# Optimization experiments

Measured on AMD Instinct MI355X. Metric: run time of the kernel, lower is better.

The kernel has to match this reference:

```python
import jax, jax.numpy as jnp
import numpy as np

EPS = 1e-5

def _ln(x, g, b):
    m = jnp.mean(x, axis=-1, keepdims=True)
    v = jnp.var(x, axis=-1, keepdims=True)
    return (x - m) / jnp.sqrt(v + EPS) * g + b

def _mha(q, k, v, Wqkv, bqkv, Wo, bo, nh):
    # torch nn.MultiheadAttention with packed in_proj: rows [0:D]=Q, [D:2D]=K, [2D:3D]=V
    D = q.shape[-1]; hd = D // nh
    qp = q @ Wqkv[:D].T + bqkv[:D]
    kp = k @ Wqkv[D:2 * D].T + bqkv[D:2 * D]
    vp = v @ Wqkv[2 * D:].T + bqkv[2 * D:]
    sh = lambda t: t.reshape(t.shape[0], t.shape[1], nh, hd).transpose(0, 2, 1, 3)
    scores = jnp.einsum('bhqd,bhkd->bhqk', sh(qp), sh(kp)) / np.float32(np.sqrt(hd))
    a = jax.nn.softmax(scores, axis=-1)
    o = jnp.einsum('bhqk,bhkd->bhqd', a, sh(vp)).transpose(0, 2, 1, 3).reshape(q.shape[0], q.shape[1], D)
    return o @ Wo.T + bo

def _forward(x, W_in, b_in, W_l, b_l, g_l, be_l, W_ih, W_hh, b_ih, b_hh, mem0,
             W_rh, b_rh, W_wh, b_wh, W_eh, b_eh, W_rg, b_rg, W_wg, b_wg,
             W_wm_qkv, b_wm_qkv, W_wm_o, b_wm_o, W_ca_qkv, b_ca_qkv, W_ca_o, b_ca_o,
             W_ai, b_ai, g_ca, be_ca, W_out, b_out):
    B, S, _ = x.shape
    H = W_in.shape[0]
    # input projection + residual MLP stack (eval mode: dropout is identity)
    h = x @ W_in.T + b_in
    for i in range(W_l.shape[0]):
        r = h
        h = _ln(jax.nn.relu(h @ W_l[i].T + b_l[i]), g_l[i], be_l[i])
        h = h + r  # use_residual=True
    # working-memory (NTM-style) scan over time
    Hd = H

    def step(carry, xt):
        hs, cs, mem = carry
        gates = xt @ W_ih.T + b_ih + hs @ W_hh.T + b_hh
        i_, f_, g_, o_ = jnp.split(gates, 4, axis=-1)  # torch LSTM gate order i,f,g,o
        cs = jax.nn.sigmoid(f_) * cs + jax.nn.sigmoid(i_) * jnp.tanh(g_)
        hs = jax.nn.sigmoid(o_) * jnp.tanh(cs)
        # read (attention over memory, then gate)
        rk = hs @ W_rh.T + b_rh
        ro = _mha(rk[:, None, :], mem, mem, W_wm_qkv, b_wm_qkv, W_wm_o, b_wm_o, 4)
        rg = jax.nn.sigmoid(hs @ W_rg.T + b_rg)  # [B,1]
        read = (rg[:, :, None] * ro)[:, 0]
        # write (erase + add with content-based addressing, unscaled bmm softmax)
        wp = hs @ W_wh.T + b_wh
        wk, wv = wp[:, :Hd], wp[:, Hd:]
        ev = jax.nn.sigmoid(hs @ W_eh.T + b_eh)
        wg = jax.nn.sigmoid(hs @ W_wg.T + b_wg)  # [B,1]
        att = jax.nn.softmax(jnp.einsum('bd,bmd->bm', wk, mem), axis=-1)
        ew = att[:, :, None]  # [B,M,1]
        mem = mem * (1.0 - ew * ev[:, None, :]) + wg[:, None, :] * (ew * wv[:, None, :])
        return (hs, cs, mem), xt + read

    mem_init = jnp.broadcast_to(mem0, (B,) + mem0.shape)
    init = (jnp.zeros((B, H), x.dtype), jnp.zeros((B, H), x.dtype), mem_init)
    _, outs = jax.lax.scan(step, init, h.transpose(1, 0, 2))
    wm = outs.transpose(1, 0, 2)  # [B,S,H]
    # cognitive attention, task_type='general' (no task modulation branch)
    att = _mha(wm, wm, wm, W_ca_qkv, b_ca_qkv, W_ca_o, b_ca_o, 8)
    inten = jax.nn.sigmoid(wm @ W_ai.T + b_ai)
    co = _ln(att * inten + wm, g_ca, be_ca)
    return co @ W_out.T + b_out

def setup_inputs():
    key = jax.random.key(0)
    ks = iter(jax.random.split(key, 40))
    B, S, DI, H, DO, L, M = 16, 512, 64, 128, 64, 3, 32
    w = lambda *s: jax.random.normal(next(ks), s, jnp.float32) * 0.05
    d = {}
    d['x'] = jax.random.normal(next(ks), (B, S, DI), jnp.float32)
    d['W_in'] = w(H, DI); d['b_in'] = jnp.zeros(H)
    d['W_l'] = w(L, H, H); d['b_l'] = jnp.zeros((L, H))
    d['g_l'] = jnp.ones((L, H)); d['be_l'] = jnp.zeros((L, H))
    d['W_ih'] = w(4 * H, H); d['W_hh'] = w(4 * H, H)
    d['b_ih'] = jnp.zeros(4 * H); d['b_hh'] = jnp.zeros(4 * H)
    d['mem0'] = w(M, H)
    d['W_rh'] = w(H, H); d['b_rh'] = jnp.zeros(H)
    d['W_wh'] = w(2 * H, H); d['b_wh'] = jnp.zeros(2 * H)
    d['W_eh'] = w(H, H); d['b_eh'] = jnp.zeros(H)
    d['W_rg'] = w(1, H); d['b_rg'] = jnp.zeros(1)
    d['W_wg'] = w(1, H); d['b_wg'] = jnp.zeros(1)
    d['W_wm_qkv'] = w(3 * H, H); d['b_wm_qkv'] = jnp.zeros(3 * H)
    d['W_wm_o'] = w(H, H); d['b_wm_o'] = jnp.zeros(H)
    d['W_ca_qkv'] = w(3 * H, H); d['b_ca_qkv'] = jnp.zeros(3 * H)
    d['W_ca_o'] = w(H, H); d['b_ca_o'] = jnp.zeros(H)
    d['W_ai'] = w(1, H); d['b_ai'] = jnp.zeros(1)
    d['g_ca'] = jnp.ones(H); d['be_ca'] = jnp.zeros(H)
    d['W_out'] = w(DO, H); d['b_out'] = jnp.zeros(DO)
    return d

def reference(x, W_in, b_in, W_l, b_l, g_l, be_l, W_ih, W_hh, b_ih, b_hh, mem0,
              W_rh, b_rh, W_wh, b_wh, W_eh, b_eh, W_rg, b_rg, W_wg, b_wg,
              W_wm_qkv, b_wm_qkv, W_wm_o, b_wm_o, W_ca_qkv, b_ca_qkv, W_ca_o, b_ca_o,
              W_ai, b_ai, g_ca, be_ca, W_out, b_out):
    return _forward(x, W_in, b_in, W_l, b_l, g_l, be_l, W_ih, W_hh, b_ih, b_hh, mem0,
                    W_rh, b_rh, W_wh, b_wh, W_eh, b_eh, W_rg, b_rg, W_wg, b_wg,
                    W_wm_qkv, b_wm_qkv, W_wm_o, b_wm_o, W_ca_qkv, b_ca_qkv, W_ca_o, b_ca_o,
                    W_ai, b_ai, g_ca, be_ca, W_out, b_out)
```

## Files before the change

### kernel.cpp

```cpp
#include <hip/hip_runtime.h>
#include <hip/hip_bf16.h>


typedef short bf16x8 __attribute__((ext_vector_type(8)));
typedef float f32x4 __attribute__((ext_vector_type(4)));
typedef float f32x16 __attribute__((ext_vector_type(16)));

__device__ __forceinline__ float bl(uint u) { return __uint_as_float(u << 16); }
__device__ __forceinline__ float bh(uint u) { return __uint_as_float(u & 0xffff0000u); }
__device__ __forceinline__ float b2f(ushort u) { return __uint_as_float(((uint)u) << 16); }
__device__ __forceinline__ ushort f2b(float f) {
  uint u = __float_as_uint(f);
  u += 0x7fffu + ((u >> 16) & 1u);
  return (ushort)(u >> 16);
}
__device__ __forceinline__ uint cvtpk(float lo, float hi) {
  uint r;
  asm("v_cvt_pk_bf16_f32 %0, %1, %2" : "=v"(r) : "v"(lo), "v"(hi));
  return r;
}
__device__ __forceinline__ float rdl(float v, int lane) {
  return __int_as_float(__builtin_amdgcn_readlane(__float_as_int(v), lane));
}
__device__ __forceinline__ float sigm(float x) { return 1.0f / (1.0f + __expf(-x)); }
__device__ __forceinline__ float tanh_(float x) { float e = __expf(2.0f * x); return 1.0f - 2.0f / (e + 1.0f); }

__device__ __forceinline__ float dppror_add(float v, const int n) {
  int s;
  switch (n) {
    case 1: s = __builtin_amdgcn_update_dpp(0, __float_as_int(v), 0x121, 0xF, 0xF, true); break;
    case 2: s = __builtin_amdgcn_update_dpp(0, __float_as_int(v), 0x122, 0xF, 0xF, true); break;
    case 4: s = __builtin_amdgcn_update_dpp(0, __float_as_int(v), 0x124, 0xF, 0xF, true); break;
    default: s = __builtin_amdgcn_update_dpp(0, __float_as_int(v), 0x128, 0xF, 0xF, true); break;
  }
  return v + __int_as_float(s);
}
__device__ __forceinline__ float dppror_max(float v, const int n) {
  int s;
  switch (n) {
    case 1: s = __builtin_amdgcn_update_dpp(0, __float_as_int(v), 0x121, 0xF, 0xF, true); break;
    case 2: s = __builtin_amdgcn_update_dpp(0, __float_as_int(v), 0x122, 0xF, 0xF, true); break;
    case 4: s = __builtin_amdgcn_update_dpp(0, __float_as_int(v), 0x124, 0xF, 0xF, true); break;
    default: s = __builtin_amdgcn_update_dpp(0, __float_as_int(v), 0x128, 0xF, 0xF, true); break;
  }
  return fmaxf(v, __int_as_float(s));
}
__device__ __forceinline__ float swap16_add(float v) {
  int a = __float_as_int(v), b = a;
  asm("v_permlane16_swap_b32 %0, %1" : "+v"(a), "+v"(b));
  return __int_as_float(a) + __int_as_float(b);
}
__device__ __forceinline__ float swap16_max(float v) {
  int a = __float_as_int(v), b = a;
  asm("v_permlane16_swap_b32 %0, %1" : "+v"(a), "+v"(b));
  return fmaxf(__int_as_float(a), __int_as_float(b));
}
__device__ __forceinline__ float fold32_add(float v) {
  int a = __float_as_int(v), b = a;
  asm("v_permlane32_swap_b32 %0, %1" : "+v"(a), "+v"(b));
  return __int_as_float(a) + __int_as_float(b);
}
__device__ __forceinline__ float qx1(float v) {
  return __int_as_float(__builtin_amdgcn_update_dpp(0, __float_as_int(v), 0xB1, 0xF, 0xF, true));
}
__device__ __forceinline__ float qx2(float v) {
  return __int_as_float(__builtin_amdgcn_update_dpp(0, __float_as_int(v), 0x4E, 0xF, 0xF, true));
}

#define O_H     ((size_t)0)
#define O_GX    ((size_t)1048576)
#define O_EW    ((size_t)1048576)
#define O_QCA   ((size_t)1048576)
#define O_KCA   ((size_t)2097152)
#define O_VCA   ((size_t)3145728)
#define O_AO    ((size_t)4194304)
#define O_WHF   ((size_t)4194304)
#define O_HS    ((size_t)5242880)
#define O_WM    ((size_t)5242880)
#define O_ST    ((size_t)6291456)
#define O_Q     ((size_t)9437184)
#define O_WGS   ((size_t)10485760)
#define O_RGS   ((size_t)10493952)
#define O_BQC   ((size_t)10502144)
#define O_MEMA  ((size_t)10502272)
#define O_PWIN  ((size_t)27279488)
#define O_PWL   ((size_t)27283584)
#define O_PWIH  ((size_t)27308160)
#define O_PCMB  ((size_t)27340928)
#define O_PQKV  ((size_t)27373696)
#define O_PWOC  ((size_t)27398272)
#define O_PWOUT ((size_t)27406464)
#define O_PWOWM ((size_t)27410688)
#define O_WQC16 ((size_t)27418880)
#define O_CAN   ((size_t)27427072)

#define F4LD(DST, OFS, P) { float4 _f = *(const float4*)(P); DST[(OFS)]=_f.x; DST[(OFS)+1]=_f.y; DST[(OFS)+2]=_f.z; DST[(OFS)+3]=_f.w; }

struct CV { const void* src; uint dst; uint n; };
struct CVA { CV d[36]; };
__global__ __launch_bounds__(256) void k_cvt(CVA a, ushort* cb)
{
  __shared__ int flag;
  int tid = threadIdx.x;
  const ushort* xu = (const ushort*)a.d[0].src;
  if (tid < 64) {
    int sane = 0;
    for (int i = tid; i < 512; i += 64) {
      int e = (xu[2 * i] >> 7) & 0xFF;
      sane += (e >= 0x70 && e <= 0x8E) ? 1 : 0;
    }
#pragma unroll
    for (int d = 1; d < 64; d <<= 1) sane += __shfl_xor(sane, d, 64);
    if (tid == 0) flag = (sane > 256) ? 0 : 1;
  }
  __syncthreads();
  int isf32 = flag;
  CV c = a.d[blockIdx.x];
  ushort* dst = cb + c.dst;
  uint start = blockIdx.y * 256 + tid, stride = gridDim.y * 256;
  if (isf32) {
    const float* s = (const float*)c.src;
    for (uint j = start; j < c.n; j += stride) dst[j] = f2b(s[j]);
  } else {
    const ushort* s = (const ushort*)c.src;
    for (uint j = start; j < c.n; j += stride) dst[j] = s[j];
  }
}

__global__ __launch_bounds__(256) void k_wqcomb(const ushort* __restrict__ Wqkv, const ushort* __restrict__ Wrh,
                                                const ushort* __restrict__ brh, const ushort* __restrict__ bqkv,
                                                ushort* __restrict__ wqc, float* __restrict__ bqc)
{
  __shared__ float qr[2][128];
  int tid = threadIdx.x;
  int r = tid >> 7, e = tid & 127;
  int j = blockIdx.x * 2 + r;
  qr[r][e] = b2f(Wqkv[j * 128 + e]);
  __syncthreads();
  float acc = 0.f;
  for (int k = 0; k < 128; ++k) acc += qr[r][k] * b2f(Wrh[k * 128 + e]);
  wqc[j * 128 + e] = f2b(acc);
  if (e == 0) {
    float s = 0.f;
    for (int k = 0; k < 128; ++k) s += qr[r][k] * b2f(brh[k]);
    bqc[j] = s + b2f(bqkv[j]);
  }
}

struct PD { const ushort* src; uint* dst; int R, C2, RT, base; };
struct PA { PD d[12]; };
__global__ __launch_bounds__(256) void k_pack(PA a)
{
  int p = blockIdx.x >> 5, sl = blockIdx.x & 31;
  PD q = a.d[p];
  for (int d2 = sl; d2 < q.C2; d2 += 32)
    for (int j = threadIdx.x; j < q.R; j += 256)
      q.dst[(size_t)d2 * q.RT + q.base + j] = *(const uint*)(q.src + (size_t)j * q.C2 * 2 + d2 * 2);
}

__global__ __launch_bounds__(256) void k_whh(const ushort* __restrict__ Whh, float* __restrict__ whf)
{
  int e = blockIdx.x * 256 + threadIdx.x;
  int j = e & 127, th = e >> 7;
  int g = j >> 5, kk = j & 31, c = th >> 2, sl = th & 3;
  whf[e] = b2f(Whh[(g * 128 + c) * 128 + sl * 32 + kk]);
}

__device__ __forceinline__ void mlp_layer(float& h0, float& h1, const uint* wp, const float* bias, int li, int l)
{
  float t0 = bias[(1 + li) * 128 + l], t1 = bias[(1 + li) * 128 + 64 + l];
#pragma unroll
  for (int d2 = 0; d2 < 64; ++d2) {
    float s0 = rdl(d2 < 32 ? h0 : h1, (2 * d2) & 63);
    float s1 = rdl(d2 < 32 ? h0 : h1, (2 * d2 + 1) & 63);
    uint u0 = wp[d2 * 128 + l], u1 = wp[d2 * 128 + 64 + l];
    t0 += s0 * bl(u0) + s1 * bh(u0);
    t1 += s0 * bl(u1) + s1 * bh(u1);
  }
  t0 = fmaxf(t0, 0.f); t1 = fmaxf(t1, 0.f);
  float sm = t0 + t1, sq = t0 * t0 + t1 * t1;
#pragma unroll
  for (int d = 1; d < 64; d <<= 1) { sm += __shfl_xor(sm, d, 64); sq += __shfl_xor(sq, d, 64); }
  float mn = sm * 0.0078125f;
  float var = sq * 0.0078125f - mn * mn;
  float rstd = rsqrtf(var + 1e-5f);
  float ng0 = bias[(4 + li) * 128 + l], ng1 = bias[(4 + li) * 128 + 64 + l];
  float nb0 = bias[(7 + li) * 128 + l], nb1 = bias[(7 + li) * 128 + 64 + l];
  h0 = (t0 - mn) * rstd * ng0 + nb0 + h0;
  h1 = (t1 - mn) * rstd * ng1 + nb1 + h1;
}

__global__ __launch_bounds__(256, 1) void k_mlp(const ushort* __restrict__ x, const uint* __restrict__ pk,
    const ushort* __restrict__ b_in, const ushort* __restrict__ b_l, const ushort* __restrict__ g_l,
    const ushort* __restrict__ be_l, float* __restrict__ h_all)
{
  __shared__ uint lds[12288];
  __shared__ float bias[1280];
  int tid = threadIdx.x;
  for (int i = tid; i < 12288; i += 256) lds[i] = pk[i];
  for (int i = tid; i < 1280; i += 256) {
    int which = i >> 7, e = i & 127;
    float v;
    if (which == 0) v = b2f(b_in[e]);
    else if (which < 4) v = b2f(b_l[(which - 1) * 128 + e]);
    else if (which < 7) v = b2f(g_l[(which - 4) * 128 + e]);
    else v = b2f(be_l[(which - 7) * 128 + e]);
    bias[i] = v;
  }
  __syncthreads();
  int wv = tid >> 6, l = tid & 63;
  float h0a[8], h1a[8];
#pragma unroll
  for (int ps = 0; ps < 8; ++ps) {
    int tok = blockIdx.x * 32 + ps * 4 + wv;
    float xv = b2f(x[(size_t)tok * 64 + l]);
    float h0 = bias[l], h1 = bias[64 + l];
#pragma unroll
    for (int d2 = 0; d2 < 32; ++d2) {
      float s0 = rdl(xv, 2 * d2), s1 = rdl(xv, 2 * d2 + 1);
      uint u0 = lds[d2 * 128 + l], u1 = lds[d2 * 128 + 64 + l];
      h0 += s0 * bl(u0) + s1 * bh(u0);
      h1 += s0 * bl(u1) + s1 * bh(u1);
    }
    mlp_layer(h0, h1, lds + 4096, bias, 0, l);
    h0a[ps] = h0; h1a[ps] = h1;
  }
  __syncthreads();
  for (int i = tid; i < 8192; i += 256) lds[i] = pk[12288 + i];
  __syncthreads();
#pragma unroll
  for (int ps = 0; ps < 8; ++ps) {
    float h0 = h0a[ps], h1 = h1a[ps];
    mlp_layer(h0, h1, lds, bias, 1, l);
    h0a[ps] = h0; h1a[ps] = h1;
  }
  __syncthreads();
  for (int i = tid; i < 8192; i += 256) lds[i] = pk[20480 + i];
  __syncthreads();
#pragma unroll
  for (int ps = 0; ps < 8; ++ps) {
    int tok = blockIdx.x * 32 + ps * 4 + wv;
    float h0 = h0a[ps], h1 = h1a[ps];
    mlp_layer(h0, h1, lds, bias, 2, l);
    h_all[(size_t)tok * 128 + l] = h0;
    h_all[(size_t)tok * 128 + 64 + l] = h1;
  }
}

__global__ __launch_bounds__(256, 1) void k_gates(const float* __restrict__ h_all, const uint* __restrict__ pk,
    const ushort* __restrict__ b_ih, const ushort* __restrict__ b_hh, float* __restrict__ gx)
{
  __shared__ uint lds[8192];
  __shared__ float biasg[512];
  int tid = threadIdx.x;
  for (int i = tid; i < 512; i += 256) biasg[i] = b2f(b_ih[i]) + b2f(b_hh[i]);
  int wv = tid >> 6, l = tid & 63;
  for (int s = 0; s < 4; ++s) {
    __syncthreads();
    for (int i = tid; i < 8192; i += 256) { int d2 = i >> 7, j = i & 127; lds[i] = pk[d2 * 512 + s * 128 + j]; }
    __syncthreads();
    for (int ps = 0; ps < 8; ++ps) {
      int tok = blockIdx.x * 32 + ps * 4 + wv;
      float h0 = h_all[(size_t)tok * 128 + l], h1 = h_all[(size_t)tok * 128 + 64 + l];
      float a0 = biasg[s * 128 + l], a1 = biasg[s * 128 + 64 + l];
#pragma unroll
      for (int d2 = 0; d2 < 64; ++d2) {
        float s0 = rdl(d2 < 32 ? h0 : h1, (2 * d2) & 63);
        float s1 = rdl(d2 < 32 ? h0 : h1, (2 * d2 + 1) & 63);
        uint u0 = lds[d2 * 128 + l], u1 = lds[d2 * 128 + 64 + l];
        a0 += s0 * bl(u0) + s1 * bh(u0);
        a1 += s0 * bl(u1) + s1 * bh(u1);
      }
      gx[(size_t)tok * 512 + s * 128 + l] = a0;
      gx[(size_t)tok * 512 + s * 128 + 64 + l] = a1;
    }
  }
}

__global__ __launch_bounds__(512, 2) void k_lstm(const float* __restrict__ gx, const float* __restrict__ whf,
                                                 float* __restrict__ hs_all)
{
  __shared__ __align__(16) float hsl[2][128];
  int tid = threadIdx.x;
  int b = blockIdx.x;
  int s = tid & 3, c = tid >> 2;
  f32x16 wA, wB, wC, wD, wE, wF, wG, wH;
  {
    const float4* wp = (const float4*)(whf + (size_t)tid * 128);
    float4 a0, a1, a2, a3;
#define LW16(V, Q) \
    a0 = wp[(Q)]; a1 = wp[(Q) + 1]; a2 = wp[(Q) + 2]; a3 = wp[(Q) + 3]; \
    V[0]=a0.x; V[1]=a0.y; V[2]=a0.z; V[3]=a0.w; V[4]=a1.x; V[5]=a1.y; V[6]=a1.z; V[7]=a1.w; \
    V[8]=a2.x; V[9]=a2.y; V[10]=a2.z; V[11]=a2.w; V[12]=a3.x; V[13]=a3.y; V[14]=a3.z; V[15]=a3.w;
    LW16(wA, 0)  LW16(wB, 4)  LW16(wC, 8)  LW16(wD, 12)
    LW16(wE, 16) LW16(wF, 20) LW16(wG, 24) LW16(wH, 28)
#undef LW16
  }
  if (tid < 128) hsl[0][tid] = 0.f;
  float cs = 0.f;
  const float* gbase = gx + (size_t)b * 512 * 512 + s * 128 + c;
  float gcur = gbase[0];
  float* hout = hs_all + (size_t)b * 512 * 128 + c;
  __syncthreads();
  for (int t = 0; t < 512; ++t) {
    float gnext = 0.f;
    if (t < 511) gnext = gbase[(size_t)(t + 1) * 512];
    const float* hp = &hsl[t & 1][s * 32];
    float p0 = (s == 0) ? gcur : 0.f;
    float p1 = (s == 1) ? gcur : 0.f;
    float p2 = (s == 2) ? gcur : 0.f;
    float p3 = (s == 3) ? gcur : 0.f;
    float4 h4;
#define DOT4(V0, V1, V2, V3, J, HOFS) \
    h4 = *(const float4*)(hp + (HOFS)); \
    p0 = fmaf(V0[(J)+0], h4.x, p0); p0 = fmaf(V0[(J)+1], h4.y, p0); p0 = fmaf(V0[(J)+2], h4.z, p0); p0 = fmaf(V0[(J)+3], h4.w, p0); \
    p1 = fmaf(V1[(J)+0], h4.x, p1); p1 = fmaf(V1[(J)+1], h4.y, p1); p1 = fmaf(V1[(J)+2], h4.z, p1); p1 = fmaf(V1[(J)+3], h4.w, p1); \
    p2 = fmaf(V2[(J)+0], h4.x, p2); p2 = fmaf(V2[(J)+1], h4.y, p2); p2 = fmaf(V2[(J)+2], h4.z, p2); p2 = fmaf(V2[(J)+3], h4.w, p2); \
    p3 = fmaf(V3[(J)+0], h4.x, p3); p3 = fmaf(V3[(J)+1], h4.y, p3); p3 = fmaf(V3[(J)+2], h4.z, p3); p3 = fmaf(V3[(J)+3], h4.w, p3);
    DOT4(wA, wC, wE, wG, 0, 0)   DOT4(wA, wC, wE, wG, 4, 4)
    DOT4(wA, wC, wE, wG, 8, 8)   DOT4(wA, wC, wE, wG, 12, 12)
    DOT4(wB, wD, wF, wH, 0, 16)  DOT4(wB, wD, wF, wH, 4, 20)
    DOT4(wB, wD, wF, wH, 8, 24)  DOT4(wB, wD, wF, wH, 12, 28)
#undef DOT4
    p0 += qx1(p0); p0 += qx2(p0);
    p1 += qx1(p1); p1 += qx2(p1);
    p2 += qx1(p2); p2 += qx2(p2);
    p3 += qx1(p3); p3 += qx2(p3);
    cs = sigm(p1) * cs + sigm(p0) * tanh_(p2);
    float hv = sigm(p3) * tanh_(cs);
    if (s == 0) {
      hsl[(t + 1) & 1][c] = hv;
      hout[(size_t)t * 128] = hv;
    }
    gcur = gnext;
    __syncthreads();
  }
}

__global__ __launch_bounds__(256, 1) void k_proj(const float* __restrict__ hs_all, const uint* __restrict__ pk,
    const ushort* __restrict__ bwh, const ushort* __restrict__ beh, const float* __restrict__ bqc,
    const ushort* __restrict__ wrg, const ushort* __restrict__ brg, const ushort* __restrict__ wwg,
    const ushort* __restrict__ bwg,
    float* __restrict__ st, float* __restrict__ q_a, float* __restrict__ rg_a)
{
  __shared__ uint lds[8192];
  __shared__ float biasc[512];
  int tid = threadIdx.x;
  for (int i = tid; i < 512; i += 256)
    biasc[i] = (i < 256) ? b2f(bwh[i]) : (i < 384) ? b2f(beh[i - 256]) : bqc[i - 384];
  float brgv = b2f(brg[0]), bwgv = b2f(bwg[0]);
  int wv = tid >> 6, l = tid & 63;
  for (int s = 0; s < 4; ++s) {
    __syncthreads();
    for (int i = tid; i < 8192; i += 256) { int d2 = i >> 7, j = i & 127; lds[i] = pk[d2 * 512 + s * 128 + j]; }
    __syncthreads();
    for (int ps = 0; ps < 8; ++ps) {
      int tok = blockIdx.x * 32 + ps * 4 + wv;
      float h0 = hs_all[(size_t)tok * 128 + l], h1 = hs_all[(size_t)tok * 128 + 64 + l];
      float a0 = biasc[s * 128 + l], a1 = biasc[s * 128 + 64 + l];
#pragma unroll
      for (int d2 = 0; d2 < 64; ++d2) {
        float s0 = rdl(d2 < 32 ? h0 : h1, (2 * d2) & 63);
        float s1 = rdl(d2 < 32 ? h0 : h1, (2 * d2 + 1) & 63);
        uint u0 = lds[d2 * 128 + l], u1 = lds[d2 * 128 + 64 + l];
        a0 += s0 * bl(u0) + s1 * bh(u0);
        a1 += s0 * bl(u1) + s1 * bh(u1);
      }
      if (s == 0) {
        st[(size_t)tok * 384 + l] = a0;
        st[(size_t)tok * 384 + 64 + l] = a1;
        float pr = h0 * b2f(wrg[l]) + h1 * b2f(wrg[64 + l]);
#pragma unroll
        for (int d = 1; d < 64; d <<= 1) pr += __shfl_xor(pr, d, 64);
        if (l == 0) rg_a[tok] = sigm(pr + brgv);
      } else if (s == 1) {
        float pw = h0 * b2f(wwg[l]) + h1 * b2f(wwg[64 + l]);
#pragma unroll
        for (int d = 1; d < 64; d <<= 1) pw += __shfl_xor(pw, d, 64);
        float wg = sigm(pw + bwgv);
        st[(size_t)tok * 384 + 256 + l] = wg * a0;
        st[(size_t)tok * 384 + 256 + 64 + l] = wg * a1;
      } else if (s == 2) {
        st[(size_t)tok * 384 + 128 + l] = sigm(a0);
        st[(size_t)tok * 384 + 128 + 64 + l] = sigm(a1);
      } else {
        q_a[(size_t)tok * 128 + l] = a0;
        q_a[(size_t)tok * 128 + 64 + l] = a1;
      }
    }
  }
}

__global__ __launch_bounds__(64, 1) void k_memrec(const float* __restrict__ st, const ushort* __restrict__ mem0,
    float* __restrict__ ew_all)
{
  __shared__ __align__(16) float sbuf[2][384];
  int l = threadIdx.x;
  int b = blockIdx.x;
  int r = l & 31, h = l >> 5;
  f32x16 mA, mB, mC, mD;
  {
    const uint* m0 = (const uint*)mem0 + r * 64 + 32 * h;
    uint4 uq;
#define LD16(V, OFS) \
    uq = *(const uint4*)(m0 + (OFS)); \
    V[0]=bl(uq.x); V[1]=bh(uq.x); V[2]=bl(uq.y); V[3]=bh(uq.y); \
    V[4]=bl(uq.z); V[5]=bh(uq.z); V[6]=bl(uq.w); V[7]=bh(uq.w); \
    uq = *(const uint4*)(m0 + (OFS) + 4); \
    V[8]=bl(uq.x); V[9]=bh(uq.x); V[10]=bl(uq.y); V[11]=bh(uq.y); \
    V[12]=bl(uq.z); V[13]=bh(uq.z); V[14]=bl(uq.w); V[15]=bh(uq.w);
    LD16(mA, 0) LD16(mB, 8) LD16(mC, 16) LD16(mD, 24)
#undef LD16
  }
  const float* stb = st + (size_t)b * 512 * 384;
  {
    float4 a = *(const float4*)(stb + 4 * l);
    float2 c = *(const float2*)(stb + 256 + 2 * l);
    *(float4*)(&sbuf[0][4 * l]) = a;
    *(float2*)(&sbuf[0][256 + 2 * l]) = c;
  }
  float4 ga1 = *(const float4*)(stb + 384 + 4 * l);
  float2 gc1 = *(const float2*)(stb + 384 + 256 + 2 * l);
  float moff = 0.f;
  float* ewp = ew_all + (size_t)b * 512 * 32 + r;
  for (int t = 0; t < 512; ++t) {
    int cur = t & 1, nxt = cur ^ 1;
    float4 ga2 = make_float4(0.f, 0.f, 0.f, 0.f);
    float2 gc2 = make_float2(0.f, 0.f);
    if (t + 2 < 512) {
      const float* sp = stb + (size_t)(t + 2) * 384;
      ga2 = *(const float4*)(sp + 4 * l);
      gc2 = *(const float2*)(sp + 256 + 2 * l);
    }
    const float* wkp = &sbuf[cur][h * 64];
    float dx = 0.f, dy = 0.f, dz = 0.f, dw = 0.f;
    float4 w4;
#define DOT4(V, J0, OFS) \
    w4 = *(const float4*)(wkp + (OFS)); \
    dx = fmaf(w4.x, V[(J0)+0], dx); dy = fmaf(w4.y, V[(J0)+1], dy); \
    dz = fmaf(w4.z, V[(J0)+2], dz); dw = fmaf(w4.w, V[(J0)+3], dw);
    DOT4(mA, 0, 0)  DOT4(mA, 4, 4)  DOT4(mA, 8, 8)   DOT4(mA, 12, 12)
    DOT4(mB, 0, 16) DOT4(mB, 4, 20) DOT4(mB, 8, 24)  DOT4(mB, 12, 28)
    DOT4(mC, 0, 32) DOT4(mC, 4, 36) DOT4(mC, 8, 40)  DOT4(mC, 12, 44)
    DOT4(mD, 0, 48) DOT4(mD, 4, 52) DOT4(mD, 8, 56)  DOT4(mD, 12, 60)
#undef DOT4
    float dp = (dx + dy) + (dz + dw);
    dp = fold32_add(dp);
    float e = __expf(dp - moff);
    float s16 = dppror_add(dppror_add(dppror_add(dppror_add(e, 1), 2), 4), 8);
    float den = swap16_add(s16);
    float ew = e * __builtin_amdgcn_rcpf(den);
    float x16 = dppror_max(dppror_max(dppror_max(dppror_max(dp, 1), 2), 4), 8);
    const float* evp = &sbuf[cur][128 + h * 64];
    const float* gvp = &sbuf[cur][256 + h * 64];
    float4 e4, g4;
#define UPD4(V, J0, OFS) \
    e4 = *(const float4*)(evp + (OFS)); g4 = *(const float4*)(gvp + (OFS)); \
    V[(J0)+0] = fmaf(ew, fmaf(-e4.x, V[(J0)+0], g4.x), V[(J0)+0]); \
    V[(J0)+1] = fmaf(ew, fmaf(-e4.y, V[(J0)+1], g4.y), V[(J0)+1]); \
    V[(J0)+2] = fmaf(ew, fmaf(-e4.z, V[(J0)+2], g4.z), V[(J0)+2]); \
    V[(J0)+3] = fmaf(ew, fmaf(-e4.w, V[(J0)+3], g4.w), V[(J0)+3]);
    UPD4(mA, 0, 0)  UPD4(mA, 4, 4)  UPD4(mA, 8, 8)   UPD4(mA, 12, 12)
    UPD4(mB, 0, 16) UPD4(mB, 4, 20) UPD4(mB, 8, 24)  UPD4(mB, 12, 28)
    UPD4(mC, 0, 32) UPD4(mC, 4, 36) UPD4(mC, 8, 40)  UPD4(mC, 12, 44)
    UPD4(mD, 0, 48) UPD4(mD, 4, 52) UPD4(mD, 8, 56)  UPD4(mD, 12, 60)
#undef UPD4
    if (t < 511) {
      *(float4*)(&sbuf[nxt][4 * l]) = ga1;
      *(float2*)(&sbuf[nxt][256 + 2 * l]) = gc1;
    }
    ga1 = ga2; gc1 = gc2;
    if (l < 32) ewp[(size_t)t * 32] = ew;
    moff = swap16_max(x16);
  }
}

__global__ __launch_bounds__(256, 1) void k_snap(const float* __restrict__ st, const float* __restrict__ ew_all,
    const ushort* __restrict__ mem0, uint* __restrict__ mem_all)
{
  int b = blockIdx.x >> 3;
  int j = ((blockIdx.x & 7) << 8) + threadIdx.x;
  int m = j >> 6, d2 = j & 63;
  uint u0 = ((const uint*)mem0)[(m << 6) + d2];
  float s0 = bl(u0), s1 = bh(u0);
  const float* ep = st + (size_t)b * 512 * 384 + 128 + 2 * d2;
  const float* gp = ep + 128;
  const float* ap = ew_all + (size_t)b * 512 * 32 + m;
  uint* mb = mem_all + (size_t)b * 512 * 2048 + (m << 6) + d2;
  for (int t = 0; t < 512; t += 4) {
    float2 eA = *(const float2*)(ep + (size_t)(t + 0) * 384);
    float2 eB = *(const float2*)(ep + (size_t)(t + 1) * 384);
    float2 eC = *(const float2*)(ep + (size_t)(t + 2) * 384);
    float2 eD = *(const float2*)(ep + (size_t)(t + 3) * 384);
    float2 gA = *(const float2*)(gp + (size_t)(t + 0) * 384);
    float2 gB = *(const float2*)(gp + (size_t)(t + 1) * 384);
    float2 gC = *(const float2*)(gp + (size_t)(t + 2) * 384);
    float2 gD = *(const float2*)(gp + (size_t)(t + 3) * 384);
    float a0 = ap[(size_t)(t + 0) * 32];
    float a1 = ap[(size_t)(t + 1) * 32];
    float a2 = ap[(size_t)(t + 2) * 32];
    float a3 = ap[(size_t)(t + 3) * 32];
    mb[(size_t)(t + 0) * 2048] = cvtpk(s0, s1);
    s0 = fmaf(a0, fmaf(-eA.x, s0, gA.x), s0);
    s1 = fmaf(a0, fmaf(-eA.y, s1, gA.y), s1);
    mb[(size_t)(t + 1) * 2048] = cvtpk(s0, s1);
    s0 = fmaf(a1, fmaf(-eB.x, s0, gB.x), s0);
    s1 = fmaf(a1, fmaf(-eB.y, s1, gB.y), s1);
    mb[(size_t)(t + 2) * 2048] = cvtpk(s0, s1);
    s0 = fmaf(a2, fmaf(-eC.x, s0, gC.x), s0);
    s1 = fmaf(a2, fmaf(-eC.y, s1, gC.y), s1);
    mb[(size_t)(t + 3) * 2048] = cvtpk(s0, s1);
    s0 = fmaf(a3, fmaf(-eD.x, s0, gD.x), s0);
    s1 = fmaf(a3, fmaf(-eD.y, s1, gD.y), s1);
  }
}

__global__ __launch_bounds__(256, 1) void k_read(const ushort* __restrict__ Wqkv, const ushort* __restrict__ bwo,
    const uint* __restrict__ wo_pk, const uint* __restrict__ mem_all, const float* __restrict__ q_all,
    const float* __restrict__ rg_all, const float* __restrict__ h_all, float* __restrict__ wm_all)
{
  __shared__ float Kl[32 * 133];
  __shared__ float Vl[32 * 133];
  __shared__ __align__(16) char ml[8192];
  __shared__ float ql[128];
  __shared__ float ol[128];
  __shared__ float part[256];
  int tid = threadIdx.x, l = tid & 63, w = tid >> 6;
  int b = blockIdx.x >> 6, c = blockIdx.x & 63;
  int mat = w >> 1, chh = w & 1;
  bf16x8 bfr[4][4];
#pragma unroll
  for (int ct = 0; ct < 4; ++ct)
#pragma unroll
    for (int kt = 0; kt < 4; ++kt) {
      int j = chh * 64 + ct * 16 + (l & 15);
      bfr[ct][kt] = *(const bf16x8*)(Wqkv + (size_t)(128 + mat * 128 + j) * 128 + kt * 32 + (l >> 4) * 8);
    }
  for (int s8 = 0; s8 < 8; ++s8) {
    int t = c * 8 + s8;
    size_t bt = (size_t)b * 512 + t;
    {
      const uint4* src = (const uint4*)(mem_all + bt * 2048);
      uint4 v0 = src[tid * 2], v1 = src[tid * 2 + 1];
      int row = tid >> 3;
      int b0 = row * 256 + (tid & 7) * 32;
      int sw = (row & 7) << 4;
      *(uint4*)(ml + (b0 ^ sw)) = v0;
      *(uint4*)(ml + ((b0 + 16) ^ sw)) = v1;
    }
    if (tid < 128) ql[tid] = q_all[bt * 128 + tid];
    __syncthreads();
    f32x4 acc[2][4];
#pragma unroll
    for (int rt = 0; rt < 2; ++rt)
#pragma unroll
      for (int ct = 0; ct < 4; ++ct) { f32x4 z = {0.f, 0.f, 0.f, 0.f}; acc[rt][ct] = z; }
    bf16x8 af[2][4];
#pragma unroll
    for (int rt = 0; rt < 2; ++rt)
#pragma unroll
      for (int kt = 0; kt < 4; ++kt) {
        int row = rt * 16 + (l & 15);
        int byte0 = (row * 256 + kt * 64 + (l >> 4) * 16) ^ ((row & 7) << 4);
        af[rt][kt] = *(const bf16x8*)(ml + byte0);
      }
#pragma unroll
    for (int rt = 0; rt < 2; ++rt)
#pragma unroll
      for (int ct = 0; ct < 4; ++ct)
#pragma unroll
        for (int kt = 0; kt < 4; ++kt)
          acc[rt][ct] = __builtin_amdgcn_mfma_f32_16x16x32_bf16(af[rt][kt], bfr[ct][kt], acc[rt][ct], 0, 0, 0);
    {
      float* dst = mat ? Vl : Kl;
#pragma unroll
      for (int rt = 0; rt < 2; ++rt)
#pragma unroll
        for (int ct = 0; ct < 4; ++ct)
#pragma unroll
          for (int rr = 0; rr < 4; ++rr) {
            int row = rt * 16 + (l >> 4) * 4 + rr;
            int col = chh * 64 + ct * 16 + (l & 15);
            dst[row * 133 + col] = acc[rt][ct][rr];
          }
    }
    __syncthreads();
    {
      int hh = w;
      float qv[16];
#pragma unroll
      for (int q = 0; q < 4; ++q) { F4LD(qv, 4 * q, ql + hh * 32 + (l >> 5) * 16 + 4 * q); }
      int m = l & 31;
      float sv = 0.f;
#pragma unroll
      for (int i = 0; i < 16; ++i) sv += qv[i] * Kl[m * 133 + hh * 32 + (l >> 5) * 16 + i];
      sv += __shfl_xor(sv, 32, 64);
      sv *= 0.1767766952966369f;
      float mx = sv;
      mx = fmaxf(mx, __shfl_xor(mx, 1, 64)); mx = fmaxf(mx, __shfl_xor(mx, 2, 64));
      mx = fmaxf(mx, __shfl_xor(mx, 4, 64)); mx = fmaxf(mx, __shfl_xor(mx, 8, 64));
      mx = fmaxf(mx, __shfl_xor(mx, 16, 64));
      float e = __expf(sv - mx);
      float den = e;
      den += __shfl_xor(den, 1, 64); den += __shfl_xor(den, 2, 64); den += __shfl_xor(den, 4, 64);
      den += __shfl_xor(den, 8, 64); den += __shfl_xor(den, 16, 64);
      float a = e / den;
      float o = 0.f;
      int dpos = l & 31, mh = l >> 5;
#pragma unroll
      for (int i = 0; i < 16; ++i) {
        int mm = mh * 16 + i;
        float am = __shfl(a, mm, 64);
        o += am * Vl[mm * 133 + hh * 32 + dpos];
      }
      o += __shfl_xor(o, 32, 64);
      if (l < 32) ol[hh * 32 + dpos] = o;
    }
    __syncthreads();
    {
      int j = tid & 127, dh = tid >> 7;
      float o0 = ol[l], o1 = ol[64 + l];
      float pa = 0.f;
#pragma unroll
      for (int i2 = 0; i2 < 32; ++i2) {
        int d2 = dh * 32 + i2;
        float s0, s1;
        if (dh == 0) { s0 = rdl(o0, 2 * i2); s1 = rdl(o0, 2 * i2 + 1); }
        else { s0 = rdl(o1, 2 * i2); s1 = rdl(o1, 2 * i2 + 1); }
        uint u = wo_pk[d2 * 128 + j];
        pa += s0 * bl(u) + s1 * bh(u);
      }
      part[tid] = pa;
    }
    __syncthreads();
    if (tid < 128) {
      float ro = part[tid] + part[tid + 128] + b2f(bwo[tid]);
      float rg = rg_all[bt];
      wm_all[bt * 128 + tid] = h_all[bt * 128 + tid] + rg * ro;
    }
    __syncthreads();
  }
}

__global__ __launch_bounds__(256, 1) void k_caqkv(const float* __restrict__ wm, const uint* __restrict__ pk,
    const ushort* __restrict__ bqkv, float* __restrict__ qca, float* __restrict__ kca, float* __restrict__ vca)
{
  __shared__ uint lds[8192];
  int tid = threadIdx.x;
  int wv = tid >> 6, l = tid & 63;
  for (int s = 0; s < 3; ++s) {
    __syncthreads();
    for (int i = tid; i < 8192; i += 256) { int d2 = i >> 7, j = i & 127; lds[i] = pk[d2 * 384 + s * 128 + j]; }
    __syncthreads();
    for (int ps = 0; ps < 8; ++ps) {
      int tok = blockIdx.x * 32 + ps * 4 + wv;
      int b = tok >> 9, ss = tok & 511;
      float h0 = wm[(size_t)tok * 128 + l], h1 = wm[(size_t)tok * 128 + 64 + l];
      float a0 = b2f(bqkv[s * 128 + l]), a1 = b2f(bqkv[s * 128 + 64 + l]);
#pragma unroll
      for (int d2 = 0; d2 < 64; ++d2) {
        float s0 = rdl(d2 < 32 ? h0 : h1, (2 * d2) & 63);
        float s1 = rdl(d2 < 32 ? h0 : h1, (2 * d2 + 1) & 63);
        uint u0 = lds[d2 * 128 + l], u1 = lds[d2 * 128 + 64 + l];
        a0 += s0 * bl(u0) + s1 * bh(u0);
        a1 += s0 * bl(u1) + s1 * bh(u1);
      }
#pragma unroll
      for (int k = 0; k < 2; ++k) {
        int j = l + 64 * k;
        int hd = j >> 4, dd = j & 15;
        size_t idx = ((size_t)(b * 8 + hd) * 512 + ss) * 16 + dd;
        float v = k == 0 ? a0 : a1;
        if (s == 0) qca[idx] = v * 0.25f;
        else if (s == 1) kca[idx] = v;
        else vca[idx] = v;
      }
    }
  }
}

__global__ __launch_bounds__(256, 1) void k_caattn(const float* __restrict__ qca, const float* __restrict__ kca,
    const float* __restrict__ vca, float* __restrict__ ao)
{
  __shared__ float kl[8192];
  __shared__ uint vl[4096];
  int tid = threadIdx.x;
  int bh_ = blockIdx.x >> 1, half = blockIdx.x & 1;
  for (int i = tid; i < 8192; i += 256) kl[i] = kca[(size_t)bh_ * 8192 + i];
  for (int i = tid; i < 4096; i += 256) {
    float v0 = vca[(size_t)bh_ * 8192 + 2 * i], v1 = vca[(size_t)bh_ * 8192 + 2 * i + 1];
    vl[i] = (uint)f2b(v0) | ((uint)f2b(v1) << 16);
  }
  __syncthreads();
  int r = half * 256 + tid;
  float qv[16];
#pragma unroll
  for (int q = 0; q < 4; ++q) { F4LD(qv, 4 * q, qca + (size_t)bh_ * 8192 + r * 16 + 4 * q); }
  float o[16];
#pragma unroll
  for (int i = 0; i < 16; ++i) o[i] = 0.f;
  float mx = -3e38f, den = 0.f;
  for (int ch = 0; ch < 8; ++ch) {
    float sc[64];
#pragma unroll
    for (int m2 = 0; m2 < 64; ++m2) {
      const float* kr = kl + (ch * 64 + m2) * 16;
      float s = 0.f;
#pragma unroll
      for (int i = 0; i < 16; ++i) s += qv[i] * kr[i];
      sc[m2] = s;
    }
    float cm = sc[0];
#pragma unroll
    for (int m2 = 1; m2 < 64; ++m2) cm = fmaxf(cm, sc[m2]);
    if (cm > mx) {
      float rs = __expf(mx - cm);
      den *= rs;
#pragma unroll
      for (int i = 0; i < 16; ++i) o[i] *= rs;
      mx = cm;
    }
#pragma unroll
    for (int m2 = 0; m2 < 64; ++m2) {
      float e = __expf(sc[m2] - mx);
      den += e;
      const uint* vr = vl + (ch * 64 + m2) * 8;
#pragma unroll
      for (int i = 0; i < 8; ++i) {
        uint u = vr[i];
        o[2 * i] += e * bl(u);
        o[2 * i + 1] += e * bh(u);
      }
    }
  }
  float rd = 1.f / den;
#pragma unroll
  for (int q = 0; q < 4; ++q) {
    float4 f = make_float4(o[4 * q] * rd, o[4 * q + 1] * rd, o[4 * q + 2] * rd, o[4 * q + 3] * rd);
    *(float4*)(ao + (size_t)bh_ * 8192 + r * 16 + 4 * q) = f;
  }
}

__global__ __launch_bounds__(256, 1) void k_cafinal(const float* __restrict__ wm, const float* __restrict__ ao,
    const uint* __restrict__ pko, const uint* __restrict__ pkout,
    const ushort* __restrict__ wai, const ushort* __restrict__ bai, const ushort* __restrict__ gca,
    const ushort* __restrict__ beca, const ushort* __restrict__ boca, const ushort* __restrict__ bout,
    float* __restrict__ out)
{
  __shared__ uint lds[12288];
  __shared__ float fb[576];
  int tid = threadIdx.x;
  for (int i = tid; i < 8192; i += 256) lds[i] = pko[i];
  for (int i = tid; i < 4096; i += 256) lds[8192 + i] = pkout[i];
  for (int i = tid; i < 576; i += 256) {
    float v;
    if (i < 128) v = b2f(wai[i]);
    else if (i < 256) v = b2f(gca[i - 128]);
    else if (i < 384) v = b2f(beca[i - 256]);
    else if (i < 512) v = b2f(boca[i - 384]);
    else v = b2f(bout[i - 512]);
    fb[i] = v;
  }
  __syncthreads();
  float baiv = b2f(bai[0]);
  int wv = tid >> 6, l = tid & 63;
  for (int ps = 0; ps < 8; ++ps) {
    int tok = blockIdx.x * 32 + ps * 4 + wv;
    int b = tok >> 9, s = tok & 511;
    float w0 = wm[(size_t)tok * 128 + l], w1 = wm[(size_t)tok * 128 + 64 + l];
    float o0 = ao[((size_t)(b * 8 + (l >> 4)) * 512 + s) * 16 + (l & 15)];
    float o1 = ao[((size_t)(b * 8 + 4 + (l >> 4)) * 512 + s) * 16 + (l & 15)];
    float ip = w0 * fb[l] + w1 * fb[64 + l];
#pragma unroll
    for (int d = 1; d < 64; d <<= 1) ip += __shfl_xor(ip, d, 64);
    float it = sigm(ip + baiv);
    float a0 = fb[384 + l], a1 = fb[384 + 64 + l];
#pragma unroll
    for (int d2 = 0; d2 < 64; ++d2) {
      float s0 = rdl(d2 < 32 ? o0 : o1, (2 * d2) & 63);
      float s1 = rdl(d2 < 32 ? o0 : o1, (2 * d2 + 1) & 63);
      uint u0 = lds[d2 * 128 + l], u1 = lds[d2 * 128 + 64 + l];
      a0 += s0 * bl(u0) + s1 * bh(u0);
      a1 += s0 * bl(u1) + s1 * bh(u1);
    }
    float x0 = a0 * it + w0, x1 = a1 * it + w1;
    float smv = x0 + x1, sq = x0 * x0 + x1 * x1;
#pragma unroll
    for (int d = 1; d < 64; d <<= 1) { smv += __shfl_xor(smv, d, 64); sq += __shfl_xor(sq, d, 64); }
    float mn = smv * 0.0078125f;
    float var = sq * 0.0078125f - mn * mn;
    float rstd = rsqrtf(var + 1e-5f);
    float c0 = (x0 - mn) * rstd * fb[128 + l] + fb[256 + l];
    float c1 = (x1 - mn) * rstd * fb[128 + 64 + l] + fb[256 + 64 + l];
    float ob = fb[512 + l];
#pragma unroll
    for (int d2 = 0; d2 < 64; ++d2) {
      float s0 = rdl(d2 < 32 ? c0 : c1, (2 * d2) & 63);
      float s1 = rdl(d2 < 32 ? c0 : c1, (2 * d2 + 1) & 63);
      uint u = lds[8192 + d2 * 64 + l];
      ob += s0 * bl(u) + s1 * bh(u);
    }
    out[(size_t)tok * 64 + l] = ob;
  }
}

extern "C" void kernel_launch(void* const* d_in, const int* in_sizes, int n_in,
                              void* d_out, int out_size, void* d_ws, size_t ws_size,
                              hipStream_t stream)
{
  (void)out_size; (void)ws_size;
  float* ws = (float*)d_ws;
  uint* wsu = (uint*)d_ws;
  ushort* cb = (ushort*)(wsu + O_CAN);

  uint off[36]; uint cum = 0;
  for (int i = 0; i < 36; ++i) { off[i] = cum; cum = (cum + (uint)in_sizes[i] + 7u) & ~7u; }

  CVA ca;
  for (int i = 0; i < 36; ++i) ca.d[i] = CV{ d_in[i], off[i], (uint)in_sizes[i] };
  k_cvt<<<dim3(36, 16), 256, 0, stream>>>(ca, cb);

  const ushort* x        = cb + off[0];
  const ushort* W_in     = cb + off[1];
  const ushort* b_in     = cb + off[2];
  const ushort* W_l      = cb + off[3];
  const ushort* b_l      = cb + off[4];
  const ushort* g_l      = cb + off[5];
  const ushort* be_l     = cb + off[6];
  const ushort* W_ih     = cb + off[7];
  const ushort* W_hh     = cb + off[8];
  const ushort* b_ih     = cb + off[9];
  const ushort* b_hh     = cb + off[10];
  const ushort* mem0     = cb + off[11];
  const ushort* W_rh     = cb + off[12];
  const ushort* b_rh     = cb + off[13];
  const ushort* W_wh     = cb + off[14];
  const ushort* b_wh     = cb + off[15];
  const ushort* W_eh     = cb + off[16];
  const ushort* b_eh     = cb + off[17];
  const ushort* W_rg     = cb + off[18];
  const ushort* b_rg     = cb + off[19];
  const ushort* W_wg     = cb + off[20];
  const ushort* b_wg     = cb + off[21];
  const ushort* W_wm_qkv = cb + off[22];
  const ushort* b_wm_qkv = cb + off[23];
  const ushort* W_wm_o   = cb + off[24];
  const ushort* b_wm_o   = cb + off[25];
  const ushort* W_ca_qkv = cb + off[26];
  const ushort* b_ca_qkv = cb + off[27];
  const ushort* W_ca_o   = cb + off[28];
  const ushort* b_ca_o   = cb + off[29];
  const ushort* W_ai     = cb + off[30];
  const ushort* b_ai     = cb + off[31];
  const ushort* g_ca     = cb + off[32];
  const ushort* be_ca    = cb + off[33];
  const ushort* W_out    = cb + off[34];
  const ushort* b_out    = cb + off[35];

  k_wqcomb<<<64, 256, 0, stream>>>(W_wm_qkv, W_rh, b_rh, b_wm_qkv, (ushort*)(wsu + O_WQC16), ws + O_BQC);

  PA pa;
  pa.d[0]  = PD{ W_in,                       wsu + O_PWIN,  128, 32, 128, 0 };
  pa.d[1]  = PD{ W_l,                        wsu + O_PWL,   128, 64, 128, 0 };
  pa.d[2]  = PD{ W_l + 16384,                wsu + O_PWL + 8192,  128, 64, 128, 0 };
  pa.d[3]  = PD{ W_l + 32768,                wsu + O_PWL + 16384, 128, 64, 128, 0 };
  pa.d[4]  = PD{ W_ih,                       wsu + O_PWIH,  512, 64, 512, 0 };
  pa.d[5]  = PD{ W_wh,                       wsu + O_PCMB,  256, 64, 512, 0 };
  pa.d[6]  = PD{ W_eh,                       wsu + O_PCMB,  128, 64, 512, 256 };
  pa.d[7]  = PD{ (const ushort*)(wsu + O_WQC16), wsu + O_PCMB, 128, 64, 512, 384 };
  pa.d[8]  = PD{ W_ca_qkv,                   wsu + O_PQKV,  384, 64, 384, 0 };
  pa.d[9]  = PD{ W_ca_o,                     wsu + O_PWOC,  128, 64, 128, 0 };
  pa.d[10] = PD{ W_out,                      wsu + O_PWOUT,  64, 64,  64, 0 };
  pa.d[11] = PD{ W_wm_o,                     wsu + O_PWOWM, 128, 64, 128, 0 };
  k_pack<<<384, 256, 0, stream>>>(pa);
  k_whh<<<256, 256, 0, stream>>>(W_hh, ws + O_WHF);

  k_mlp<<<256, 256, 0, stream>>>(x, wsu + O_PWIN, b_in, b_l, g_l, be_l, ws + O_H);
  k_gates<<<256, 256, 0, stream>>>(ws + O_H, wsu + O_PWIH, b_ih, b_hh, ws + O_GX);
  k_lstm<<<16, 512, 0, stream>>>(ws + O_GX, ws + O_WHF, ws + O_HS);
  k_proj<<<256, 256, 0, stream>>>(ws + O_HS, wsu + O_PCMB, b_wh, b_eh, ws + O_BQC,
                                  W_rg, b_rg, W_wg, b_wg,
                                  ws + O_ST, ws + O_Q, ws + O_RGS);
  k_memrec<<<16, 64, 0, stream>>>(ws + O_ST, mem0, ws + O_EW);
  k_snap<<<128, 256, 0, stream>>>(ws + O_ST, ws + O_EW, mem0, wsu + O_MEMA);
  k_read<<<1024, 256, 0, stream>>>(W_wm_qkv, b_wm_o, wsu + O_PWOWM, wsu + O_MEMA,
                                   ws + O_Q, ws + O_RGS, ws + O_H, ws + O_WM);
  k_caqkv<<<256, 256, 0, stream>>>(ws + O_WM, wsu + O_PQKV, b_ca_qkv, ws + O_QCA, ws + O_KCA, ws + O_VCA);
  k_caattn<<<256, 256, 0, stream>>>(ws + O_QCA, ws + O_KCA, ws + O_VCA, ws + O_AO);
  k_cafinal<<<256, 256, 0, stream>>>(ws + O_WM, ws + O_AO, wsu + O_PWOC, wsu + O_PWOUT,
                                     W_ai, b_ai, g_ca, be_ca, b_ca_o, b_out, (float*)d_out);
}
```

Baseline: 1.358 ms.

## Defer memory update to shorten serial dependency chain in memory recurrence

Restructures the per-step memory recurrence so the next step's dot product is built from two partial dots, one over the not-yet-updated memory and one over the erase/add delta vector. The scalar combine dp = A - ew*D then depends on the previous softmax weight only through a single FMA. The full memory update is deferred, so the long dot-product reduction no longer sits on the softmax critical path. In exchange it doubles the register state (a delta vector per memory element), adds extra FMAs per step, and changes the floating-point rounding order.

Result: slower. 1.450 ms (+6.7%).

```diff
diff --git a/kernel.cpp b/kernel.cpp
--- a/kernel.cpp
+++ b/kernel.cpp
@@ -399,6 +399,7 @@
   int b = blockIdx.x;
   int r = l & 31, h = l >> 5;
   f32x16 mA, mB, mC, mD;
+  f32x16 eA, eB, eC, eD;
   {
     const uint* m0 = (const uint*)mem0 + r * 64 + 32 * h;
     uint4 uq;
@@ -412,6 +413,10 @@
     LD16(mA, 0) LD16(mB, 8) LD16(mC, 16) LD16(mD, 24)
 #undef LD16
   }
+  {
+    f32x16 z = {0.f,0.f,0.f,0.f,0.f,0.f,0.f,0.f,0.f,0.f,0.f,0.f,0.f,0.f,0.f,0.f};
+    eA = z; eB = z; eC = z; eD = z;
+  }
   const float* stb = st + (size_t)b * 512 * 384;
   {
     float4 a = *(const float4*)(stb + 4 * l);
@@ -421,10 +426,29 @@
   }
   float4 ga1 = *(const float4*)(stb + 384 + 4 * l);
   float2 gc1 = *(const float2*)(stb + 384 + 256 + 2 * l);
-  float moff = 0.f;
-  float* ewp = ew_all + (size_t)b * 512 * 32 + r;
+  float A, D = 0.f, ewp = 0.f, moff = 0.f;
+  {
+    const float* wkp = &sbuf[0][h * 64];
+    float ax = 0.f, ay = 0.f, az = 0.f, aw = 0.f;
+    float4 w4;
+#define DOTP(V, J0, OFS) \
+    w4 = *(const float4*)(wkp + (OFS)); \
+    ax = fmaf(w4.x, V[(J0)+0], ax); ay = fmaf(w4.y, V[(J0)+1], ay); \
+    az = fmaf(w4.z, V[(J0)+2], az); aw = fmaf(w4.w, V[(J0)+3], aw);
+    DOTP(mA, 0, 0)  DOTP(mA, 4, 4)  DOTP(mA, 8, 8)   DOTP(mA, 12, 12)
+    DOTP(mB, 0, 16) DOTP(mB, 4, 20) DOTP(mB, 8, 24)  DOTP(mB, 12, 28)
+    DOTP(mC, 0, 32) DOTP(mC, 4, 36) DOTP(mC, 8, 40)  DOTP(mC, 12, 44)
+    DOTP(mD, 0, 48) DOTP(mD, 4, 52) DOTP(mD, 8, 56)  DOTP(mD, 12, 60)
+#undef DOTP
+    A = (ax + ay) + (az + aw);
+  }
+  float* ewo = ew_all + (size_t)b * 512 * 32 + r;
   for (int t = 0; t < 512; ++t) {
     int cur = t & 1, nxt = cur ^ 1;
+    if (t < 511) {
+      *(float4*)(&sbuf[nxt][4 * l]) = ga1;
+      *(float2*)(&sbuf[nxt][256 + 2 * l]) = gc1;
+    }
     float4 ga2 = make_float4(0.f, 0.f, 0.f, 0.f);
     float2 gc2 = make_float2(0.f, 0.f);
     if (t + 2 < 512) {
@@ -432,46 +456,58 @@
       ga2 = *(const float4*)(sp + 4 * l);
       gc2 = *(const float2*)(sp + 256 + 2 * l);
     }
-    const float* wkp = &sbuf[cur][h * 64];
-    float dx = 0.f, dy = 0.f, dz = 0.f, dw = 0.f;
-    float4 w4;
-#define DOT4(V, J0, OFS) \
-    w4 = *(const float4*)(wkp + (OFS)); \
-    dx = fmaf(w4.x, V[(J0)+0], dx); dy = fmaf(w4.y, V[(J0)+1], dy); \
-    dz = fmaf(w4.z, V[(J0)+2], dz); dw = fmaf(w4.w, V[(J0)+3], dw);
-    DOT4(mA, 0, 0)  DOT4(mA, 4, 4)  DOT4(mA, 8, 8)   DOT4(mA, 12, 12)
-    DOT4(mB, 0, 16) DOT4(mB, 4, 20) DOT4(mB, 8, 24)  DOT4(mB, 12, 28)
-    DOT4(mC, 0, 32) DOT4(mC, 4, 36) DOT4(mC, 8, 40)  DOT4(mC, 12, 44)
-    DOT4(mD, 0, 48) DOT4(mD, 4, 52) DOT4(mD, 8, 56)  DOT4(mD, 12, 60)
-#undef DOT4
-    float dp = (dx + dy) + (dz + dw);
-    dp = fold32_add(dp);
+    float dp = fold32_add(fmaf(-ewp, D, A));
     float e = __expf(dp - moff);
     float s16 = dppror_add(dppror_add(dppror_add(dppror_add(e, 1), 2), 4), 8);
     float den = swap16_add(s16);
     float ew = e * __builtin_amdgcn_rcpf(den);
     float x16 = dppror_max(dppror_max(dppror_max(dppror_max(dp, 1), 2), 4), 8);
+    if (l < 32) ewo[(size_t)t * 32] = ew;
+#define ADV16(MV, EV) \
+    MV[0]=fmaf(-ewp,EV[0],MV[0]);   MV[1]=fmaf(-ewp,EV[1],MV[1]); \
+    MV[2]=fmaf(-ewp,EV[2],MV[2]);   MV[3]=fmaf(-ewp,EV[3],MV[3]); \
+    MV[4]=fmaf(-ewp,EV[4],MV[4]);   MV[5]=fmaf(-ewp,EV[5],MV[5]); \
+    MV[6]=fmaf(-ewp,EV[6],MV[6]);   MV[7]=fmaf(-ewp,EV[7],MV[7]); \
+    MV[8]=fmaf(-ewp,EV[8],MV[8]);   MV[9]=fmaf(-ewp,EV[9],MV[9]); \
+    MV[10]=fmaf(-ewp,EV[10],MV[10]); MV[11]=fmaf(-ewp,EV[11],MV[11]); \
+    MV[12]=fmaf(-ewp,EV[12],MV[12]); MV[13]=fmaf(-ewp,EV[13],MV[13]); \
+    MV[14]=fmaf(-ewp,EV[14],MV[14]); MV[15]=fmaf(-ewp,EV[15],MV[15]);
+    ADV16(mA, eA) ADV16(mB, eB) ADV16(mC, eC) ADV16(mD, eD)
+#undef ADV16
     const float* evp = &sbuf[cur][128 + h * 64];
     const float* gvp = &sbuf[cur][256 + h * 64];
     float4 e4, g4;
-#define UPD4(V, J0, OFS) \
+#define EM4(MV, EV, J, OFS) \
     e4 = *(const float4*)(evp + (OFS)); g4 = *(const float4*)(gvp + (OFS)); \
-    V[(J0)+0] = fmaf(ew, fmaf(-e4.x, V[(J0)+0], g4.x), V[(J0)+0]); \
-    V[(J0)+1] = fmaf(ew, fmaf(-e4.y, V[(J0)+1], g4.y), V[(J0)+1]); \
-    V[(J0)+2] = fmaf(ew, fmaf(-e4.z, V[(J0)+2], g4.z), V[(J0)+2]); \
-    V[(J0)+3] = fmaf(ew, fmaf(-e4.w, V[(J0)+3], g4.w), V[(J0)+3]);
-    UPD4(mA, 0, 0)  UPD4(mA, 4, 4)  UPD4(mA, 8, 8)   UPD4(mA, 12, 12)
-    UPD4(mB, 0, 16) UPD4(mB, 4, 20) UPD4(mB, 8, 24)  UPD4(mB, 12, 28)
-    UPD4(mC, 0, 32) UPD4(mC, 4, 36) UPD4(mC, 8, 40)  UPD4(mC, 12, 44)
-    UPD4(mD, 0, 48) UPD4(mD, 4, 52) UPD4(mD, 8, 56)  UPD4(mD, 12, 60)
-#undef UPD4
-    if (t < 511) {
-      *(float4*)(&sbuf[nxt][4 * l]) = ga1;
-      *(float2*)(&sbuf[nxt][256 + 2 * l]) = gc1;
-    }
+    EV[(J)+0] = fmaf(e4.x, MV[(J)+0], -g4.x); \
+    EV[(J)+1] = fmaf(e4.y, MV[(J)+1], -g4.y); \
+    EV[(J)+2] = fmaf(e4.z, MV[(J)+2], -g4.z); \
+    EV[(J)+3] = fmaf(e4.w, MV[(J)+3], -g4.w);
+    EM4(mA, eA, 0, 0)  EM4(mA, eA, 4, 4)  EM4(mA, eA, 8, 8)   EM4(mA, eA, 12, 12)
+    EM4(mB, eB, 0, 16) EM4(mB, eB, 4, 20) EM4(mB, eB, 8, 24)  EM4(mB, eB, 12, 28)
+    EM4(mC, eC, 0, 32) EM4(mC, eC, 4, 36) EM4(mC, eC, 8, 40)  EM4(mC, eC, 12, 44)
+    EM4(mD, eD, 0, 48) EM4(mD, eD, 4, 52) EM4(mD, eD, 8, 56)  EM4(mD, eD, 12, 60)
+#undef EM4
+    const float* wkn = &sbuf[nxt][h * 64];
+    float ax = 0.f, ay = 0.f, az = 0.f, aw = 0.f;
+    float dxx = 0.f, dyy = 0.f, dzz = 0.f, dww = 0.f;
+    float4 w4;
+#define AD4(MV, EV, J, OFS) \
+    w4 = *(const float4*)(wkn + (OFS)); \
+    ax = fmaf(w4.x, MV[(J)+0], ax); dxx = fmaf(w4.x, EV[(J)+0], dxx); \
+    ay = fmaf(w4.y, MV[(J)+1], ay); dyy = fmaf(w4.y, EV[(J)+1], dyy); \
+    az = fmaf(w4.z, MV[(J)+2], az); dzz = fmaf(w4.z, EV[(J)+2], dzz); \
+    aw = fmaf(w4.w, MV[(J)+3], aw); dww = fmaf(w4.w, EV[(J)+3], dww);
+    AD4(mA, eA, 0, 0)  AD4(mA, eA, 4, 4)  AD4(mA, eA, 8, 8)   AD4(mA, eA, 12, 12)
+    AD4(mB, eB, 0, 16) AD4(mB, eB, 4, 20) AD4(mB, eB, 8, 24)  AD4(mB, eB, 12, 28)
+    AD4(mC, eC, 0, 32) AD4(mC, eC, 4, 36) AD4(mC, eC, 8, 40)  AD4(mC, eC, 12, 44)
+    AD4(mD, eD, 0, 48) AD4(mD, eD, 4, 52) AD4(mD, eD, 8, 56)  AD4(mD, eD, 12, 60)
+#undef AD4
+    A = (ax + ay) + (az + aw);
+    D = (dxx + dyy) + (dzz + dww);
+    ewp = ew;
+    moff = swap16_max(x16);
     ga1 = ga2; gc1 = gc2;
-    if (l < 32) ewp[(size_t)t * 32] = ew;
-    moff = swap16_max(x16);
   }
 }
 
```
